# Optimization experiments

Hardware: AMD Instinct MI355X
Metric: run time of the kernel (lower is better)

## Reference

```python
import jax, jax.numpy as jnp
import numpy as np

NUM_GRAPHS = 128

def setup_inputs() -> dict:
    key = jax.random.key(0)
    k1, k2, k3, k4, k5, k6 = jax.random.split(key, 6)
    N, E, H = 100000, 3200000, 256
    x = jax.random.normal(k1, (N, 1), dtype=jnp.float32)
    edge_index = jax.random.randint(k2, (2, E), 0, N, dtype=jnp.int64)
    batch = jnp.sort(jax.random.randint(k3, (N,), 0, NUM_GRAPHS, dtype=jnp.int64))
    # SAGEConv lin_l: [in=1 -> out=H], plus bias; final Linear [H -> 1]
    W_l = jax.random.normal(k4, (1, H), dtype=jnp.float32) / jnp.sqrt(1.0)
    b_l = jnp.zeros((H,), dtype=jnp.float32)
    W_out = jax.random.normal(k5, (H, 1), dtype=jnp.float32) / jnp.sqrt(H)
    b_out = jax.random.normal(k6, (1,), dtype=jnp.float32) * 0.01
    return {"x": x, "edge_index": edge_index, "batch": batch,
            "W_l": W_l, "b_l": b_l, "W_out": W_out, "b_out": b_out}

def reference(x, edge_index, batch, W_l, b_l, W_out, b_out):
    N = x.shape[0]
    src, dst = edge_index[0], edge_index[1]
    # SAGEConv(aggr='sum', root_weight=False): agg[i] = sum_{j->i} x[j]; out = agg @ W_l + b_l
    agg = jax.ops.segment_sum(x[src], dst, num_segments=N)  # [N,1]
    h = agg @ W_l + b_l                                      # [N,H]
    h = jax.nn.relu(h)
    # global_mean_pool over batch ids
    sums = jax.ops.segment_sum(h, batch, num_segments=NUM_GRAPHS)          # [G,H]
    counts = jax.ops.segment_sum(jnp.ones((N,), h.dtype), batch, num_segments=NUM_GRAPHS)
    pooled = sums / jnp.maximum(counts, 1.0)[:, None]
    out = pooled @ W_out + b_out                             # [G,1]
    return jax.nn.relu(out)
```

## Files before the change

kernel.cpp:

```cpp
#include <hip/hip_runtime.h>


#define GMAX  128
#define HMAX  256
#define BS    256
#define NBMAX 512
#define SG    512


__global__ __launch_bounds__(256) void s1_count(const int* __restrict__ ei,
                                                unsigned* __restrict__ cnt,
                                                int E, int NB, int QpB) {
  __shared__ unsigned h[NBMAX];
  int tid = threadIdx.x;
  for (int b = tid; b < NB; b += 256) h[b] = 0u;
  __syncthreads();
  int Q = E >> 2;
  int q0 = blockIdx.x * QpB;
  int q1 = min(q0 + QpB, Q);
  const int4* d4 = (const int4*)(ei + E);
  for (int q = q0 + tid; q < q1; q += 256) {
    int4 d = d4[q];
    atomicAdd(&h[d.x >> 8], 1u);
    atomicAdd(&h[d.y >> 8], 1u);
    atomicAdd(&h[d.z >> 8], 1u);
    atomicAdd(&h[d.w >> 8], 1u);
  }
  if (blockIdx.x == 0)
    for (int e = (Q << 2) + tid; e < E; e += 256)
      atomicAdd(&h[ei[E + e] >> 8], 1u);
  __syncthreads();
  for (int b = tid; b < NB; b += 256) cnt[(size_t)b * SG + blockIdx.x] = h[b];
}

__global__ __launch_bounds__(SG) void s_scanA(const unsigned* __restrict__ cnt,
                                              unsigned* __restrict__ off,
                                              unsigned* __restrict__ tot) {
  __shared__ unsigned s[SG];
  int b = blockIdx.x, t = threadIdx.x;
  unsigned c = cnt[(size_t)b * SG + t];
  s[t] = c;
  __syncthreads();
  for (int o = 1; o < SG; o <<= 1) {
    unsigned v = (t >= o) ? s[t - o] : 0u;
    __syncthreads();
    s[t] += v;
    __syncthreads();
  }
  off[(size_t)b * SG + t] = s[t] - c;
  if (t == SG - 1) tot[b] = s[t];
}

__global__ __launch_bounds__(NBMAX) void s_scanB(const unsigned* __restrict__ tot,
                                                 unsigned* __restrict__ base, int NB) {
  __shared__ unsigned s[NBMAX];
  int t = threadIdx.x;
  unsigned c = (t < NB) ? ((tot[t] + 3u) & ~3u) : 0u;
  s[t] = c;
  __syncthreads();
  for (int o = 1; o < NBMAX; o <<= 1) {
    unsigned v = (t >= o) ? s[t - o] : 0u;
    __syncthreads();
    s[t] += v;
    __syncthreads();
  }
  if (t < NB) base[t] = s[t] - c;
}

__global__ __launch_bounds__(256) void s2_scatter(const int* __restrict__ ei,
                                                  const unsigned* __restrict__ off,
                                                  const unsigned* __restrict__ base,
                                                  unsigned* __restrict__ pairs,
                                                  int E, int NB, int QpB) {
  __shared__ unsigned hb[NBMAX];
  __shared__ unsigned rcur[NBMAX];
  int tid = threadIdx.x;
  for (int b = tid; b < NB; b += 256) {
    hb[b] = base[b] + off[(size_t)b * SG + blockIdx.x];
    rcur[b] = 0u;
  }
  __syncthreads();
  int Q = E >> 2;
  int q0 = blockIdx.x * QpB;
  int q1 = min(q0 + QpB, Q);
  const int4* s4 = (const int4*)ei;
  const int4* d4 = (const int4*)(ei + E);
  for (int q = q0 + tid; q < q1; q += 256) {
    int4 s = s4[q];
    int4 d = d4[q];
    { int b = d.x >> 8; unsigned r = atomicAdd(&rcur[b], 1u);
      pairs[hb[b] + r] = ((unsigned)s.x << 8) | (unsigned)(d.x & 255); }
    { int b = d.y >> 8; unsigned r = atomicAdd(&rcur[b], 1u);
      pairs[hb[b] + r] = ((unsigned)s.y << 8) | (unsigned)(d.y & 255); }
    { int b = d.z >> 8; unsigned r = atomicAdd(&rcur[b], 1u);
      pairs[hb[b] + r] = ((unsigned)s.z << 8) | (unsigned)(d.z & 255); }
    { int b = d.w >> 8; unsigned r = atomicAdd(&rcur[b], 1u);
      pairs[hb[b] + r] = ((unsigned)s.w << 8) | (unsigned)(d.w & 255); }
  }
  if (blockIdx.x == 0)
    for (int e = (Q << 2) + tid; e < E; e += 256) {
      int d = ei[E + e], s = ei[e];
      int b = d >> 8; unsigned r = atomicAdd(&rcur[b], 1u);
      pairs[hb[b] + r] = ((unsigned)s << 8) | (unsigned)(d & 255);
    }
}

__global__ __launch_bounds__(256) void s3_reduce(
    const unsigned* __restrict__ pairs, const unsigned* __restrict__ base,
    const unsigned* __restrict__ tot,
    const float* __restrict__ x, const int* __restrict__ batch,
    const float* __restrict__ Wl, const float* __restrict__ bl,
    const float* __restrict__ Wo,
    float* __restrict__ gsum, float* __restrict__ gcnt, int N, int H) {
  __shared__ float acc[BS];
  __shared__ float sWl[HMAX], sbl[HMAX], sWo[HMAX];
  __shared__ float ls[GMAX], lc[GMAX];
  int tid = threadIdx.x, b = blockIdx.x;
  acc[tid] = 0.f;
  if (tid < H) { sWl[tid] = Wl[tid]; sbl[tid] = bl[tid]; sWo[tid] = Wo[tid]; }
  if (tid < GMAX) { ls[tid] = 0.f; lc[tid] = 0.f; }
  __syncthreads();

  unsigned lo = base[b], cnt = tot[b];
  unsigned q4 = cnt >> 2;
  const uint4* p4 = (const uint4*)(pairs + lo);
  for (unsigned i = tid; i < q4; i += 256) {
    uint4 p = p4[i];
    atomicAdd(&acc[p.x & 255u], x[p.x >> 8]);
    atomicAdd(&acc[p.y & 255u], x[p.y >> 8]);
    atomicAdd(&acc[p.z & 255u], x[p.z >> 8]);
    atomicAdd(&acc[p.w & 255u], x[p.w >> 8]);
  }
  if (tid < (int)(cnt & 3u)) {
    unsigned p = pairs[lo + (q4 << 2) + tid];
    atomicAdd(&acc[p & 255u], x[p >> 8]);
  }
  __syncthreads();

  int node = b * BS + tid;
  if (node < N) {
    float a = acc[tid], f = 0.f;
#pragma unroll 8
    for (int k = 0; k < H; ++k) {
      float hh = fmaf(a, sWl[k], sbl[k]);
      f = fmaf(fmaxf(hh, 0.f), sWo[k], f);
    }
    int g = batch[node];
    atomicAdd(&ls[g], f);
    atomicAdd(&lc[g], 1.f);
  }
  __syncthreads();
  if (tid < GMAX && lc[tid] != 0.f) {
    atomicAdd(&gsum[tid], ls[tid]);
    atomicAdd(&gcnt[tid], lc[tid]);
  }
}

__global__ void final_kernel(const float* __restrict__ gsum,
                             const float* __restrict__ gcnt,
                             const float* __restrict__ b_out,
                             float* __restrict__ out, int G) {
  int g = blockIdx.x * blockDim.x + threadIdx.x;
  if (g < G) {
    float c = fmaxf(gcnt[g], 1.f);
    out[g] = fmaxf(gsum[g] / c + b_out[0], 0.f);
  }
}


__global__ __launch_bounds__(256) void fb_scatter(const int* __restrict__ ei,
                                                  const float* __restrict__ x,
                                                  float* __restrict__ agg, int E) {
  int t = blockIdx.x * blockDim.x + threadIdx.x;
  if (t < E) atomicAdd(&agg[ei[E + t]], x[ei[t]]);
}

__global__ __launch_bounds__(256) void fb_node(const float* __restrict__ agg,
                                               const int* __restrict__ batch,
                                               const float* __restrict__ Wl,
                                               const float* __restrict__ bl,
                                               const float* __restrict__ Wo,
                                               float* __restrict__ gsum,
                                               float* __restrict__ gcnt, int N, int H) {
  __shared__ float sWl[HMAX], sbl[HMAX], sWo[HMAX];
  __shared__ float ls[GMAX], lc[GMAX];
  int tid = threadIdx.x;
  if (tid < H) { sWl[tid] = Wl[tid]; sbl[tid] = bl[tid]; sWo[tid] = Wo[tid]; }
  if (tid < GMAX) { ls[tid] = 0.f; lc[tid] = 0.f; }
  __syncthreads();
  int i = blockIdx.x * blockDim.x + tid;
  if (i < N) {
    float a = agg[i], f = 0.f;
    for (int k = 0; k < H; ++k) {
      float hh = fmaf(a, sWl[k], sbl[k]);
      f = fmaf(fmaxf(hh, 0.f), sWo[k], f);
    }
    int g = batch[i];
    atomicAdd(&ls[g], f);
    atomicAdd(&lc[g], 1.f);
  }
  __syncthreads();
  if (tid < GMAX && lc[tid] != 0.f) {
    atomicAdd(&gsum[tid], ls[tid]);
    atomicAdd(&gcnt[tid], lc[tid]);
  }
}


extern "C" void kernel_launch(void* const* d_in, const int* in_sizes, int n_in,
                              void* d_out, int out_size, void* d_ws, size_t ws_size,
                              hipStream_t stream) {
  const float* x     = (const float*)d_in[0];
  const int*   ei    = (const int*)d_in[1];
  const int*   batch = (const int*)d_in[2];
  const float* Wl    = (const float*)d_in[3];
  const float* bl    = (const float*)d_in[4];
  const float* Wo    = (const float*)d_in[5];
  const float* bo    = (const float*)d_in[6];
  float* out = (float*)d_out;

  int N = in_sizes[0];
  int E = in_sizes[1] / 2;
  int H = in_sizes[3];
  int G = out_size;

  int NB = (N + BS - 1) / BS;
  int Q  = E >> 2;
  int QpB = (Q + SG - 1) / SG;

  const size_t W_CNT  = (size_t)NBMAX * SG;
  const size_t W_OFF  = W_CNT;
  const size_t HDRW   = W_CNT + W_OFF + 2 * NBMAX + 2 * GMAX;
  size_t need = (HDRW + (size_t)E + 3u * (size_t)NB) * 4u;

  unsigned* w = (unsigned*)d_ws;
  if (NB <= NBMAX && ws_size >= need && H <= HMAX && G <= GMAX) {
    unsigned* cnt   = w;
    unsigned* off   = cnt + W_CNT;
    unsigned* tot   = off + W_OFF;
    unsigned* base  = tot + NBMAX;
    float*    gsum  = (float*)(base + NBMAX);
    float*    gcnt  = gsum + GMAX;
    unsigned* pairs = (unsigned*)(gcnt + GMAX);

    hipMemsetAsync(gsum, 0, 2u * GMAX * sizeof(float), stream);
    s1_count<<<SG, 256, 0, stream>>>(ei, cnt, E, NB, QpB);
    s_scanA<<<NB, SG, 0, stream>>>(cnt, off, tot);
    s_scanB<<<1, NBMAX, 0, stream>>>(tot, base, NB);
    s2_scatter<<<SG, 256, 0, stream>>>(ei, off, base, pairs, E, NB, QpB);
    s3_reduce<<<NB, 256, 0, stream>>>(pairs, base, tot, x, batch,
                                      Wl, bl, Wo, gsum, gcnt, N, H);
    final_kernel<<<1, 128, 0, stream>>>(gsum, gcnt, bo, out, G);
  } else {
    float* agg  = (float*)d_ws;
    float* gsum = agg + N;
    float* gcnt = gsum + GMAX;
    hipMemsetAsync(d_ws, 0, ((size_t)N + 2 * GMAX) * 4u, stream);
    fb_scatter<<<(E + 255) / 256, 256, 0, stream>>>(ei, x, agg, E);
    fb_node<<<(N + 255) / 256, 256, 0, stream>>>(agg, batch, Wl, bl, Wo,
                                                 gsum, gcnt, N, H);
    final_kernel<<<1, 128, 0, stream>>>(gsum, gcnt, bo, out, G);
  }
}
```

Baseline: 147.5 us.

## Use fixed-capacity buckets, drop second scan, fold memset and final into kernels

```diff
diff --git a/kernel.cpp b/kernel.cpp
--- a/kernel.cpp
+++ b/kernel.cpp
@@ -5,7 +5,7 @@
 #define HMAX  256
 #define BS    256
 #define NBMAX 512
-#define SG    512
+#define SG    1024
 
 
 __global__ __launch_bounds__(256) void s1_count(const int* __restrict__ ei,
@@ -30,15 +30,19 @@
     for (int e = (Q << 2) + tid; e < E; e += 256)
       atomicAdd(&h[ei[E + e] >> 8], 1u);
   __syncthreads();
-  for (int b = tid; b < NB; b += 256) cnt[(size_t)b * SG + blockIdx.x] = h[b];
-}
-
-__global__ __launch_bounds__(SG) void s_scanA(const unsigned* __restrict__ cnt,
-                                              unsigned* __restrict__ off,
-                                              unsigned* __restrict__ tot) {
+  for (int b = tid; b < NB; b += 256)
+    cnt[(size_t)blockIdx.x * NBMAX + b] = h[b];
+}
+
+__global__ __launch_bounds__(SG) void s_scan(const unsigned* __restrict__ cnt,
+                                             unsigned* __restrict__ off,
+                                             unsigned* __restrict__ tot,
+                                             float* __restrict__ gsum,
+                                             float* __restrict__ gcnt,
+                                             unsigned* __restrict__ done) {
   __shared__ unsigned s[SG];
   int b = blockIdx.x, t = threadIdx.x;
-  unsigned c = cnt[(size_t)b * SG + t];
+  unsigned c = cnt[(size_t)t * NBMAX + b];
   s[t] = c;
   __syncthreads();
   for (int o = 1; o < SG; o <<= 1) {
@@ -47,36 +51,23 @@
     s[t] += v;
     __syncthreads();
   }
-  off[(size_t)b * SG + t] = s[t] - c;
+  off[(size_t)t * NBMAX + b] = s[t] - c;
   if (t == SG - 1) tot[b] = s[t];
-}
-
-__global__ __launch_bounds__(NBMAX) void s_scanB(const unsigned* __restrict__ tot,
-                                                 unsigned* __restrict__ base, int NB) {
-  __shared__ unsigned s[NBMAX];
-  int t = threadIdx.x;
-  unsigned c = (t < NB) ? ((tot[t] + 3u) & ~3u) : 0u;
-  s[t] = c;
-  __syncthreads();
-  for (int o = 1; o < NBMAX; o <<= 1) {
-    unsigned v = (t >= o) ? s[t - o] : 0u;
-    __syncthreads();
-    s[t] += v;
-    __syncthreads();
-  }
-  if (t < NB) base[t] = s[t] - c;
+  if (b == 0) {
+    if (t < GMAX) { gsum[t] = 0.f; gcnt[t] = 0.f; }
+    if (t == 0) done[0] = 0u;
+  }
 }
 
 __global__ __launch_bounds__(256) void s2_scatter(const int* __restrict__ ei,
                                                   const unsigned* __restrict__ off,
-                                                  const unsigned* __restrict__ base,
                                                   unsigned* __restrict__ pairs,
-                                                  int E, int NB, int QpB) {
+                                                  int E, int NB, int QpB, int CAP) {
   __shared__ unsigned hb[NBMAX];
   __shared__ unsigned rcur[NBMAX];
   int tid = threadIdx.x;
   for (int b = tid; b < NB; b += 256) {
-    hb[b] = base[b] + off[(size_t)b * SG + blockIdx.x];
+    hb[b] = (unsigned)b * (unsigned)CAP + off[(size_t)blockIdx.x * NBMAX + b];
     rcur[b] = 0u;
   }
   __syncthreads();
@@ -85,43 +76,57 @@
   int q1 = min(q0 + QpB, Q);
   const int4* s4 = (const int4*)ei;
   const int4* d4 = (const int4*)(ei + E);
+  unsigned capu = (unsigned)CAP;
   for (int q = q0 + tid; q < q1; q += 256) {
     int4 s = s4[q];
     int4 d = d4[q];
     { int b = d.x >> 8; unsigned r = atomicAdd(&rcur[b], 1u);
-      pairs[hb[b] + r] = ((unsigned)s.x << 8) | (unsigned)(d.x & 255); }
+      unsigned slot = hb[b] + r;
+      if (slot < (unsigned)(b + 1) * capu)
+        pairs[slot] = ((unsigned)s.x << 8) | (unsigned)(d.x & 255); }
     { int b = d.y >> 8; unsigned r = atomicAdd(&rcur[b], 1u);
-      pairs[hb[b] + r] = ((unsigned)s.y << 8) | (unsigned)(d.y & 255); }
+      unsigned slot = hb[b] + r;
+      if (slot < (unsigned)(b + 1) * capu)
+        pairs[slot] = ((unsigned)s.y << 8) | (unsigned)(d.y & 255); }
     { int b = d.z >> 8; unsigned r = atomicAdd(&rcur[b], 1u);
-      pairs[hb[b] + r] = ((unsigned)s.z << 8) | (unsigned)(d.z & 255); }
+      unsigned slot = hb[b] + r;
+      if (slot < (unsigned)(b + 1) * capu)
+        pairs[slot] = ((unsigned)s.z << 8) | (unsigned)(d.z & 255); }
     { int b = d.w >> 8; unsigned r = atomicAdd(&rcur[b], 1u);
-      pairs[hb[b] + r] = ((unsigned)s.w << 8) | (unsigned)(d.w & 255); }
+      unsigned slot = hb[b] + r;
+      if (slot < (unsigned)(b + 1) * capu)
+        pairs[slot] = ((unsigned)s.w << 8) | (unsigned)(d.w & 255); }
   }
   if (blockIdx.x == 0)
     for (int e = (Q << 2) + tid; e < E; e += 256) {
       int d = ei[E + e], s = ei[e];
       int b = d >> 8; unsigned r = atomicAdd(&rcur[b], 1u);
-      pairs[hb[b] + r] = ((unsigned)s << 8) | (unsigned)(d & 255);
+      unsigned slot = hb[b] + r;
+      if (slot < (unsigned)(b + 1) * capu)
+        pairs[slot] = ((unsigned)s << 8) | (unsigned)(d & 255);
     }
 }
 
 __global__ __launch_bounds__(256) void s3_reduce(
-    const unsigned* __restrict__ pairs, const unsigned* __restrict__ base,
-    const unsigned* __restrict__ tot,
+    const unsigned* __restrict__ pairs, const unsigned* __restrict__ tot,
     const float* __restrict__ x, const int* __restrict__ batch,
     const float* __restrict__ Wl, const float* __restrict__ bl,
-    const float* __restrict__ Wo,
-    float* __restrict__ gsum, float* __restrict__ gcnt, int N, int H) {
+    const float* __restrict__ Wo, const float* __restrict__ b_out,
+    float* __restrict__ gsum, float* __restrict__ gcnt,
+    unsigned* __restrict__ done, float* __restrict__ out,
+    int N, int H, int G, int CAP) {
   __shared__ float acc[BS];
   __shared__ float sWl[HMAX], sbl[HMAX], sWo[HMAX];
   __shared__ float ls[GMAX], lc[GMAX];
+  __shared__ unsigned ticket;
   int tid = threadIdx.x, b = blockIdx.x;
   acc[tid] = 0.f;
   if (tid < H) { sWl[tid] = Wl[tid]; sbl[tid] = bl[tid]; sWo[tid] = Wo[tid]; }
   if (tid < GMAX) { ls[tid] = 0.f; lc[tid] = 0.f; }
   __syncthreads();
 
-  unsigned lo = base[b], cnt = tot[b];
+  unsigned lo = (unsigned)b * (unsigned)CAP;
+  unsigned cnt = min(tot[b], (unsigned)CAP);
   unsigned q4 = cnt >> 2;
   const uint4* p4 = (const uint4*)(pairs + lo);
   for (unsigned i = tid; i < q4; i += 256) {
@@ -154,16 +159,14 @@
     atomicAdd(&gsum[tid], ls[tid]);
     atomicAdd(&gcnt[tid], lc[tid]);
   }
-}
-
-__global__ void final_kernel(const float* __restrict__ gsum,
-                             const float* __restrict__ gcnt,
-                             const float* __restrict__ b_out,
-                             float* __restrict__ out, int G) {
-  int g = blockIdx.x * blockDim.x + threadIdx.x;
-  if (g < G) {
-    float c = fmaxf(gcnt[g], 1.f);
-    out[g] = fmaxf(gsum[g] / c + b_out[0], 0.f);
+  __threadfence();
+  __syncthreads();
+  if (tid == 0) ticket = atomicAdd(done, 1u);
+  __syncthreads();
+  if (ticket == gridDim.x - 1 && tid < G) {
+    float s = __hip_atomic_load(&gsum[tid], __ATOMIC_RELAXED, __HIP_MEMORY_SCOPE_AGENT);
+    float c = __hip_atomic_load(&gcnt[tid], __ATOMIC_RELAXED, __HIP_MEMORY_SCOPE_AGENT);
+    out[tid] = fmaxf(s / fmaxf(c, 1.f) + b_out[0], 0.f);
   }
 }
 
@@ -206,6 +209,14 @@
   }
 }
 
+__global__ void fb_final(const float* __restrict__ gsum,
+                         const float* __restrict__ gcnt,
+                         const float* __restrict__ b_out,
+                         float* __restrict__ out, int G) {
+  int g = blockIdx.x * blockDim.x + threadIdx.x;
+  if (g < G) out[g] = fmaxf(gsum[g] / fmaxf(gcnt[g], 1.f) + b_out[0], 0.f);
+}
+
 
 extern "C" void kernel_launch(void* const* d_in, const int* in_sizes, int n_in,
                               void* d_out, int out_size, void* d_ws, size_t ws_size,
@@ -225,32 +236,32 @@
   int G = out_size;
 
   int NB = (N + BS - 1) / BS;
-  int Q  = E >> 2;
+  int Q   = E >> 2;
   int QpB = (Q + SG - 1) / SG;
 
-  const size_t W_CNT  = (size_t)NBMAX * SG;
-  const size_t W_OFF  = W_CNT;
-  const size_t HDRW   = W_CNT + W_OFF + 2 * NBMAX + 2 * GMAX;
-  size_t need = (HDRW + (size_t)E + 3u * (size_t)NB) * 4u;
+  int avg = (NB > 0) ? E / NB : 0;
+  int CAP = (2 * avg + 4095) & ~4095;
+  if (CAP < 4096) CAP = 4096;
+
+  const size_t W_MAT = (size_t)SG * NBMAX;
+  const size_t HDRW  = 2 * W_MAT + NBMAX + 2 * GMAX + 4;
+  size_t need = (HDRW + (size_t)NB * (size_t)CAP) * 4u;
 
   unsigned* w = (unsigned*)d_ws;
-  if (NB <= NBMAX && ws_size >= need && H <= HMAX && G <= GMAX) {
+  if (NB <= NBMAX && ws_size >= need && H <= HMAX && G <= GMAX && G <= 256) {
     unsigned* cnt   = w;
-    unsigned* off   = cnt + W_CNT;
-    unsigned* tot   = off + W_OFF;
-    unsigned* base  = tot + NBMAX;
-    float*    gsum  = (float*)(base + NBMAX);
+    unsigned* off   = cnt + W_MAT;
+    unsigned* tot   = off + W_MAT;
+    float*    gsum  = (float*)(tot + NBMAX);
     float*    gcnt  = gsum + GMAX;
-    unsigned* pairs = (unsigned*)(gcnt + GMAX);
-
-    hipMemsetAsync(gsum, 0, 2u * GMAX * sizeof(float), stream);
+    unsigned* done  = (unsigned*)(gcnt + GMAX);
+    unsigned* pairs = done + 4;
+
     s1_count<<<SG, 256, 0, stream>>>(ei, cnt, E, NB, QpB);
-    s_scanA<<<NB, SG, 0, stream>>>(cnt, off, tot);
-    s_scanB<<<1, NBMAX, 0, stream>>>(tot, base, NB);
-    s2_scatter<<<SG, 256, 0, stream>>>(ei, off, base, pairs, E, NB, QpB);
-    s3_reduce<<<NB, 256, 0, stream>>>(pairs, base, tot, x, batch,
-                                      Wl, bl, Wo, gsum, gcnt, N, H);
-    final_kernel<<<1, 128, 0, stream>>>(gsum, gcnt, bo, out, G);
+    s_scan<<<NB, SG, 0, stream>>>(cnt, off, tot, gsum, gcnt, done);
+    s2_scatter<<<SG, 256, 0, stream>>>(ei, off, pairs, E, NB, QpB, CAP);
+    s3_reduce<<<NB, 256, 0, stream>>>(pairs, tot, x, batch, Wl, bl, Wo, bo,
+                                      gsum, gcnt, done, out, N, H, G, CAP);
   } else {
     float* agg  = (float*)d_ws;
     float* gsum = agg + N;
@@ -259,6 +270,6 @@
     fb_scatter<<<(E + 255) / 256, 256, 0, stream>>>(ei, x, agg, E);
     fb_node<<<(N + 255) / 256, 256, 0, stream>>>(agg, batch, Wl, bl, Wo,
                                                  gsum, gcnt, N, H);
-    final_kernel<<<1, 128, 0, stream>>>(gsum, gcnt, bo, out, G);
-  }
-}
+    fb_final<<<1, 256, 0, stream>>>(gsum, gcnt, bo, out, G);
+  }
+}
```

Result: slower. 174.1 us (+18.0%).
